# Kernel tuning notes

Measured on AMD Instinct MI355X. Metric: run time of the kernel, lower is better.

Reference implementation:

```python
import jax, jax.numpy as jnp
import numpy as np

DIM = 768
N_HEAD = 12
HEAD_DIM = 64
INNER = N_HEAD * HEAD_DIM
SCALE = HEAD_DIM ** -0.5


def setup_inputs() -> dict:
    key = jax.random.key(0)
    ks = jax.random.split(key, 12)
    B, Sf, St = 4, 2048, 2048
    from_tensor = jax.random.normal(ks[0], (B, Sf, DIM), dtype=jnp.float32)
    to_tensor = jax.random.normal(ks[1], (B, St, DIM), dtype=jnp.float32)
    attention_mask = jax.random.randint(ks[2], (B, Sf, St), 0, 2, dtype=jnp.int32)
    # Dense layers: kernel ~ RandomNormal (stddev 0.05, keras default), bias zeros
    def kern(k, fan_in, fan_out):
        return 0.05 * jax.random.normal(k, (fan_in, fan_out), dtype=jnp.float32)
    return {
        "from_tensor": from_tensor,
        "to_tensor": to_tensor,
        "attention_mask": attention_mask,
        "Wq": kern(ks[3], DIM, INNER), "bq": jnp.zeros((INNER,), jnp.float32),
        "Wk": kern(ks[4], DIM, INNER), "bk": jnp.zeros((INNER,), jnp.float32),
        "Wv": kern(ks[5], DIM, INNER), "bv": jnp.zeros((INNER,), jnp.float32),
        "Wo": kern(ks[6], INNER, DIM), "bo": jnp.zeros((DIM,), jnp.float32),
    }


def reference(from_tensor, to_tensor, attention_mask, Wq, bq, Wk, bk, Wv, bv, Wo, bo):
    B, Sf, _ = from_tensor.shape
    St = to_tensor.shape[1]
    # projections -> [B, S, n_head, head_dim] -> [B, n_head, S, head_dim]
    def split_heads(x, S):
        return x.reshape(B, S, N_HEAD, HEAD_DIM).transpose(0, 2, 1, 3)
    q = split_heads(from_tensor @ Wq + bq, Sf) * SCALE
    k = split_heads(to_tensor @ Wk + bk, St)
    v = split_heads(to_tensor @ Wv + bv, St)
    # scores [B, H, Sf, St]
    scores = jnp.einsum('bhik,bhjk->bhij', q, k)
    adder = (1.0 - attention_mask.astype(jnp.float32)) * -10000.0
    scores = scores + adder[:, None, :, :]
    probs = jax.nn.softmax(scores, axis=-1)
    out = jnp.einsum('bhij,bhjk->bhik', probs, v)  # [B, H, Sf, Dh]
    out = out.transpose(0, 2, 1, 3).reshape(B, Sf, INNER)
    return out @ Wo + bo
```

## Files before the change

### kernel.cpp

```cpp
#include <hip/hip_runtime.h>
#include <stdint.h>

#define DIM 768
#define NH 12
#define HD 64
#define BSZ 4
#define SEQ 2048
#define MROWS (BSZ*SEQ)

typedef __attribute__((ext_vector_type(8))) short v8s;
typedef __attribute__((ext_vector_type(4))) float v4f;
typedef __attribute__((ext_vector_type(8))) _Float16 v8h;
typedef __attribute__((ext_vector_type(2))) __fp16 v2fp;

__device__ __forceinline__ uint16_t f2bf(float x) {
  union { float f; uint32_t u; } v; v.f = x;
  uint32_t r = v.u + 0x7fffu + ((v.u >> 16) & 1u);
  return (uint16_t)(r >> 16);
}

#if __has_builtin(__builtin_amdgcn_cvt_pk_bf16_f32)
typedef __attribute__((ext_vector_type(2))) __bf16 v2bf;
__device__ __forceinline__ uint32_t pack_bf16(float a, float b) {
  union { v2bf v; uint32_t u; } c;
  c.v = __builtin_amdgcn_cvt_pk_bf16_f32(a, b);
  return c.u;
}
#else
__device__ __forceinline__ uint32_t pack_bf16(float a, float b) {
  return (uint32_t)f2bf(a) | ((uint32_t)f2bf(b) << 16);
}
#endif

__device__ __forceinline__ uint32_t pack_f16(float a, float b) {
#if __has_builtin(__builtin_amdgcn_cvt_pkrtz)
  union { v2fp h; uint32_t u; } c;
  c.h = __builtin_amdgcn_cvt_pkrtz(a, b);
  return c.u;
#else
  union { _Float16 h[2]; uint32_t u; } c;
  c.h[0] = (_Float16)a; c.h[1] = (_Float16)b; return c.u;
#endif
}

__device__ __forceinline__ float fexp2(float x) {
#if __has_builtin(__builtin_amdgcn_exp2f)
  return __builtin_amdgcn_exp2f(x);
#else
  return exp2f(x);
#endif
}

__device__ __forceinline__ void gl16(const void* g, void* l) {
  __builtin_amdgcn_global_load_lds(
      (const __attribute__((address_space(1))) unsigned int*)g,
      (__attribute__((address_space(3))) unsigned int*)l, 16, 0, 0);
}

__global__ void cvt_bf16_kernel(const float* __restrict__ src0, uint16_t* __restrict__ dst0,
                                const float* __restrict__ src1, uint16_t* __restrict__ dst1,
                                int n4) {
  int i = blockIdx.x * blockDim.x + threadIdx.x;
  const float* src = (i < n4) ? src0 : src1;
  uint16_t* dst = (i < n4) ? dst0 : dst1;
  int j = (i < n4) ? i : i - n4;
  float4 v = ((const float4*)src)[j];
  ushort4 o;
  o.x = f2bf(v.x); o.y = f2bf(v.y); o.z = f2bf(v.z); o.w = f2bf(v.w);
  ((ushort4*)dst)[j] = o;
}

__global__ void mask_bits_kernel(const int* __restrict__ src,
                                 unsigned long long* __restrict__ dst, int nwords) {
  int gtid = blockIdx.x * blockDim.x + threadIdx.x;
  int w = gtid >> 6;
  int lane = threadIdx.x & 63;
  if (w >= nwords) return;
  int b  = w >> 16;
  int q  = (w >> 5) & 2047;
  int kt = w & 31;
  int m = src[((size_t)b * SEQ + q) * SEQ + kt * 64 + lane];
  unsigned long long bits = __ballot(m != 0);
  if (lane == 0) dst[((size_t)b * 32 + kt) * SEQ + q] = bits;
}

__global__ void wtrans_kernel(const float* __restrict__ Wq, const float* __restrict__ Wk,
                              const float* __restrict__ Wv, const float* __restrict__ Wo,
                              uint16_t* __restrict__ WT) {
  __shared__ float tile[32][33];
  int z = blockIdx.z;
  const float* src = (z==0) ? Wq : (z==1) ? Wk : (z==2) ? Wv : Wo;
  uint16_t* dst = WT + (size_t)z * DIM * DIM;
  int tx = threadIdx.x, ty = threadIdx.y;
  int x  = blockIdx.x * 32 + tx;
  int y0 = blockIdx.y * 32;
  for (int j = ty; j < 32; j += 8)
    tile[j][tx] = src[(size_t)(y0 + j) * DIM + x];
  __syncthreads();
  int xo = y0 + tx;
  for (int j = ty; j < 32; j += 8)
    dst[(size_t)(blockIdx.x * 32 + j) * DIM + xo] = f2bf(tile[tx][j]);
}

__global__ __launch_bounds__(256) void gemm_kernel(
    const uint16_t* __restrict__ Xf, const uint16_t* __restrict__ Xt,
    const uint16_t* __restrict__ WT, const uint16_t* __restrict__ AO,
    const float* __restrict__ bq, const float* __restrict__ bk,
    const float* __restrict__ bv, const float* __restrict__ bo,
    uint16_t* __restrict__ Qw, uint16_t* __restrict__ Kw, uint16_t* __restrict__ Vw,
    float* __restrict__ Out, int mode_base)
{
  __shared__ alignas(16) uint16_t As[128 * 32];
  __shared__ alignas(16) uint16_t Bs[128 * 32];
  int mode = mode_base + blockIdx.z;
  const uint16_t* A = (mode == 0) ? Xf : (mode == 3 ? AO : Xt);
  const uint16_t* W = WT + (size_t)mode * DIM * DIM;
  const float* bias = (mode == 0) ? bq : (mode == 1) ? bk : (mode == 2) ? bv : bo;

  int m0 = blockIdx.x * 128, n0 = blockIdx.y * 128;
  int tid = threadIdx.x;
  int wave = tid >> 6, lane = tid & 63, lr = lane & 15, quad = lane >> 4;
  int wm = (wave >> 1) * 64, wn = (wave & 1) * 64;

  int seg = (lane & 3) ^ ((lane >> 3) & 3);
  const uint16_t* agl = A + (size_t)(m0 + wave * 32 + (lane >> 2)) * DIM + seg * 8;
  const uint16_t* bgl = W + (size_t)(n0 + wave * 32 + (lane >> 2)) * DIM + seg * 8;
  int lb = wave * 1024;
  int ck = (lr >> 1) & 3;

  v4f acc[4][4];
  v4f vz = {0.f, 0.f, 0.f, 0.f};
  #pragma unroll
  for (int i = 0; i < 4; i++)
    #pragma unroll
    for (int j = 0; j < 4; j++) acc[i][j] = vz;

  for (int k0 = 0; k0 < DIM; k0 += 32) {
    __syncthreads();
    gl16(agl + k0,            &As[lb]);
    gl16(agl + k0 + 16 * DIM, &As[lb + 512]);
    gl16(bgl + k0,            &Bs[lb]);
    gl16(bgl + k0 + 16 * DIM, &Bs[lb + 512]);
    __syncthreads();
    v8s af[4], bfr[4];
    #pragma unroll
    for (int i = 0; i < 4; i++)
      af[i] = *(const v8s*)&As[(wm + i * 16 + lr) * 32 + ((quad ^ ck) << 3)];
    #pragma unroll
    for (int j = 0; j < 4; j++)
      bfr[j] = *(const v8s*)&Bs[(wn + j * 16 + lr) * 32 + ((quad ^ ck) << 3)];
    #pragma unroll
    for (int i = 0; i < 4; i++)
      #pragma unroll
      for (int j = 0; j < 4; j++)
        acc[i][j] = __builtin_amdgcn_mfma_f32_16x16x32_bf16(af[i], bfr[j], acc[i][j], 0, 0, 0);
  }

  float bj[4];
  #pragma unroll
  for (int j = 0; j < 4; j++) bj[j] = bias[n0 + wn + j * 16 + lr];

  if (mode == 3) {
    #pragma unroll
    for (int i = 0; i < 4; i++) {
      int m = m0 + wm + i * 16 + quad * 4;
      #pragma unroll
      for (int j = 0; j < 4; j++) {
        int n = n0 + wn + j * 16 + lr;
        #pragma unroll
        for (int r = 0; r < 4; r++)
          Out[(size_t)(m + r) * DIM + n] = acc[i][j][r] + bj[j];
      }
    }
  } else if (mode == 2) {
    #pragma unroll
    for (int i = 0; i < 4; i++) {
      int m = m0 + wm + i * 16 + quad * 4;
      int b = m >> 11, s0 = m & 2047;
      int kk0 = s0 & 63;
      int pos = (kk0 >> 5) * 32 + ((kk0 >> 2) & 3) * 8 + ((kk0 >> 4) & 1) * 4;
      int chunk = pos >> 3, off = pos & 7;
      #pragma unroll
      for (int j = 0; j < 4; j++) {
        int n = n0 + wn + j * 16 + lr;
        int h = n >> 6, d = n & 63;
        uint2 pk;
        pk.x = pack_f16(acc[i][j][0] + bj[j], acc[i][j][1] + bj[j]);
        pk.y = pack_f16(acc[i][j][2] + bj[j], acc[i][j][3] + bj[j]);
        int idx = (s0 & ~63) + ((chunk ^ (d & 7)) << 3) + off;
        *(uint2*)&Vw[((size_t)(b * NH + h) * HD + d) * SEQ + idx] = pk;
      }
    }
  } else {
    uint16_t* Dst = (mode == 0) ? Qw : Kw;
    float scale = (mode == 0) ? 0.18033688f : 1.0f;
    #pragma unroll
    for (int i = 0; i < 4; i++) {
      int m = m0 + wm + i * 16 + quad * 4;
      int b = m >> 11, s0 = m & 2047;
      #pragma unroll
      for (int j = 0; j < 4; j++) {
        int n = n0 + wn + j * 16 + lr;
        int h = n >> 6, d = n & 63;
        #pragma unroll
        for (int r = 0; r < 4; r++) {
          float v = (acc[i][j][r] + bj[j]) * scale;
          int s = s0 + r;
          int dd = (mode == 1) ? ((((d >> 3) ^ (s & 7)) << 3) + (d & 7)) : d;
          Dst[((size_t)(b * NH + h) * SEQ + s) * HD + dd] = f2bf(v);
        }
      }
    }
  }
}

__device__ __forceinline__ void softmax8(unsigned long long mw, int sh0,
                                         const v4f* s, v8h* pf, float& lsum) {
  uint32_t mlo = (uint32_t)mw, mhi = (uint32_t)(mw >> 32);
  #pragma unroll
  for (int p = 0; p < 2; p++) {
    float ps[8];
    #pragma unroll
    for (int half = 0; half < 2; half++) {
      int nt = p * 2 + half;
      uint32_t b4 = ((nt < 2 ? mlo : mhi) >> (sh0 + ((nt & 1) << 4))) & 15u;
      #pragma unroll
      for (int r = 0; r < 4; r++) {
        float v = fexp2(s[nt][r] - 8.0f) * (float)((b4 >> r) & 1u);
        ps[half * 4 + r] = v;
        lsum += v;
      }
    }
    union { uint4 u; v8h h; } cc;
    cc.u.x = pack_f16(ps[0], ps[1]);
    cc.u.y = pack_f16(ps[2], ps[3]);
    cc.u.z = pack_f16(ps[4], ps[5]);
    cc.u.w = pack_f16(ps[6], ps[7]);
    pf[p] = cc.h;
  }
}

__global__ __launch_bounds__(128, 3) void flash_kernel(
    const uint16_t* __restrict__ Qg, const uint16_t* __restrict__ Kg,
    const uint16_t* __restrict__ Vg, const unsigned long long* __restrict__ Mb,
    uint16_t* __restrict__ AO)
{
  __shared__ alignas(16) uint16_t Ks[64 * 64];
  __shared__ alignas(16) uint16_t Vs[64 * 64];

  int tid = threadIdx.x, wave = tid >> 6, lane = tid & 63, lr = lane & 15, quad = lane >> 4;
  int bh = blockIdx.y;
  int b = bh / NH, h = bh - b * NH;
  int q0 = blockIdx.x * 64;
  const uint16_t* Qp = Qg + (size_t)bh * SEQ * HD;
  const uint16_t* Kp = Kg + (size_t)bh * SEQ * HD;
  const uint16_t* Vp = Vg + (size_t)bh * HD * SEQ;
  int qg0 = q0 + wave * 32 + lr;
  int qg1 = qg0 + 16;
  const unsigned long long* Mp0 = Mb + (size_t)b * 32 * SEQ + qg0;
  const unsigned long long* Mp1 = Mp0 + 16;

  int swk = lr & 7, sh0 = quad * 4;

  v8s qf0a = *(const v8s*)&Qp[(size_t)qg0 * HD + quad * 8];
  v8s qf0b = *(const v8s*)&Qp[(size_t)qg0 * HD + 32 + quad * 8];
  v8s qf1a = *(const v8s*)&Qp[(size_t)qg1 * HD + quad * 8];
  v8s qf1b = *(const v8s*)&Qp[(size_t)qg1 * HD + 32 + quad * 8];

  const uint16_t* kgl = Kp + ((size_t)(wave * 32 + (lane >> 3)) * HD + (lane & 7) * 8);
  const uint16_t* vgl = Vp + ((size_t)(wave * 32 + (lane >> 3)) * SEQ + (lane & 7) * 8);
  int lb = wave * 2048;

  v4f acc0[4], acc1[4];
  v4f vz = {0.f, 0.f, 0.f, 0.f};
  #pragma unroll
  for (int dt = 0; dt < 4; dt++) { acc0[dt] = vz; acc1[dt] = vz; }
  float ls0 = 0.f, ls1 = 0.f;

  for (int k0 = 0; k0 < SEQ; k0 += 64) {
    __syncthreads();
    #pragma unroll
    for (int c = 0; c < 4; c++) {
      gl16(kgl + ((size_t)k0 + c * 8) * HD, &Ks[lb + c * 512]);
      gl16(vgl + k0 + (size_t)c * 8 * SEQ, &Vs[lb + c * 512]);
    }
    unsigned long long mw0 = Mp0[(size_t)(k0 >> 6) * SEQ];
    unsigned long long mw1 = Mp1[(size_t)(k0 >> 6) * SEQ];
    __syncthreads();

    v4f s0[4], s1[4];
    #pragma unroll
    for (int nt = 0; nt < 4; nt++) {
      int rowb = (nt * 16 + lr) << 6;
      v8s kf0 = *(const v8s*)&Ks[rowb + ((quad ^ swk) << 3)];
      v8s kf1 = *(const v8s*)&Ks[rowb + (((quad + 4) ^ swk) << 3)];
      v4f z = vz;
      z = __builtin_amdgcn_mfma_f32_16x16x32_bf16(kf0, qf0a, z, 0, 0, 0);
      z = __builtin_amdgcn_mfma_f32_16x16x32_bf16(kf1, qf0b, z, 0, 0, 0);
      s0[nt] = z;
      z = vz;
      z = __builtin_amdgcn_mfma_f32_16x16x32_bf16(kf0, qf1a, z, 0, 0, 0);
      z = __builtin_amdgcn_mfma_f32_16x16x32_bf16(kf1, qf1b, z, 0, 0, 0);
      s1[nt] = z;
    }

    v8h pf0[2], pf1[2];
    softmax8(mw0, sh0, s0, pf0, ls0);
    softmax8(mw1, sh0, s1, pf1, ls1);

    #pragma unroll
    for (int dt = 0; dt < 4; dt++) {
      int rowb = (dt * 16 + lr) << 6;
      #pragma unroll
      for (int p = 0; p < 2; p++) {
        v8h vv = *(const v8h*)&Vs[rowb + (((p * 4 + quad) ^ swk) << 3)];
        acc0[dt] = __builtin_amdgcn_mfma_f32_16x16x32_f16(vv, pf0[p], acc0[dt], 0, 0, 0);
        acc1[dt] = __builtin_amdgcn_mfma_f32_16x16x32_f16(vv, pf1[p], acc1[dt], 0, 0, 0);
      }
    }
  }

  ls0 += __shfl_xor(ls0, 16); ls0 += __shfl_xor(ls0, 32);
  ls1 += __shfl_xor(ls1, 16); ls1 += __shfl_xor(ls1, 32);
  float ri0 = 1.0f / ls0, ri1 = 1.0f / ls1;

  #pragma unroll
  for (int dt = 0; dt < 4; dt++) {
    uint2 pk;
    pk.x = pack_bf16(acc0[dt][0] * ri0, acc0[dt][1] * ri0);
    pk.y = pack_bf16(acc0[dt][2] * ri0, acc0[dt][3] * ri0);
    *(uint2*)&AO[(size_t)(b * SEQ + qg0) * DIM + h * HD + dt * 16 + sh0] = pk;
    pk.x = pack_bf16(acc1[dt][0] * ri1, acc1[dt][1] * ri1);
    pk.y = pack_bf16(acc1[dt][2] * ri1, acc1[dt][3] * ri1);
    *(uint2*)&AO[(size_t)(b * SEQ + qg1) * DIM + h * HD + dt * 16 + sh0] = pk;
  }
}

extern "C" void kernel_launch(void* const* d_in, const int* in_sizes, int n_in,
                              void* d_out, int out_size, void* d_ws, size_t ws_size,
                              hipStream_t stream) {
  const float* from_t = (const float*)d_in[0];
  const float* to_t   = (const float*)d_in[1];
  const int*   maski  = (const int*)d_in[2];
  const float* Wq = (const float*)d_in[3];  const float* bq = (const float*)d_in[4];
  const float* Wk = (const float*)d_in[5];  const float* bk = (const float*)d_in[6];
  const float* Wv = (const float*)d_in[7];  const float* bv = (const float*)d_in[8];
  const float* Wo = (const float*)d_in[9];  const float* bo = (const float*)d_in[10];

  char* ws = (char*)d_ws;
  size_t off = 0;
  uint16_t* Xf = (uint16_t*)(ws + off); off += (size_t)MROWS * DIM * 2;
  uint16_t* Xt = (uint16_t*)(ws + off); off += (size_t)MROWS * DIM * 2;
  uint16_t* WT = (uint16_t*)(ws + off); off += (size_t)4 * DIM * DIM * 2;
  unsigned long long* Mbits = (unsigned long long*)(ws + off);
  off += (size_t)BSZ * 32 * SEQ * 8;
  uint16_t* Qw = (uint16_t*)(ws + off); off += (size_t)MROWS * DIM * 2;
  uint16_t* Kw = (uint16_t*)(ws + off); off += (size_t)MROWS * DIM * 2;
  uint16_t* Vw = (uint16_t*)(ws + off); off += (size_t)MROWS * DIM * 2;
  uint16_t* AO = (uint16_t*)(ws + off); off += (size_t)MROWS * DIM * 2;
  float* Out = (float*)d_out;

  int nx4 = MROWS * DIM / 4;
  cvt_bf16_kernel<<<2 * nx4 / 256, 256, 0, stream>>>(from_t, Xf, to_t, Xt, nx4);
  int nwords = BSZ * 32 * SEQ;
  mask_bits_kernel<<<nwords * 64 / 256, 256, 0, stream>>>(maski, Mbits, nwords);
  wtrans_kernel<<<dim3(24, 24, 4), dim3(32, 8), 0, stream>>>(Wq, Wk, Wv, Wo, WT);

  gemm_kernel<<<dim3(64, 6, 3), 256, 0, stream>>>(Xf, Xt, WT, AO, bq, bk, bv, bo,
                                                  Qw, Kw, Vw, Out, 0);
  flash_kernel<<<dim3(SEQ / 64, BSZ * NH), 128, 0, stream>>>(Qw, Kw, Vw, Mbits, AO);
  gemm_kernel<<<dim3(64, 6, 1), 256, 0, stream>>>(Xf, Xt, WT, AO, bq, bk, bv, bo,
                                                  Qw, Kw, Vw, Out, 3);
}
```

Before: 329.3 us.

## Transpose GEMM MFMA for vectorized epilogue stores and move row-sum to MFMA

Q/K and output projections swap MFMA operand order so each lane holds four consecutive columns, enabling float4 output stores and packed bf16 stores instead of scalar writes; the V projection is split into its own kernel keeping the old layout. In the flash kernel, the mask is applied via sign-extended bitfield AND instead of a float multiply, the softmax row sum is computed by an extra MFMA against a ones vector instead of scalar adds and shuffles, the next mask word is prefetched a tile ahead, and LDS offsets are hoisted. The prefetch reads one word past the end, so the mask workspace is enlarged; the extra MFMAs add matrix-core work.

```diff
diff --git a/kernel.cpp b/kernel.cpp
--- a/kernel.cpp
+++ b/kernel.cpp
@@ -49,6 +49,17 @@
 #else
   return exp2f(x);
 #endif
+}
+
+__device__ __forceinline__ int sbfe1(uint32_t w, int off) {
+#if __has_builtin(__builtin_amdgcn_sbfe)
+  return __builtin_amdgcn_sbfe((int)w, off, 1);
+#else
+  return ((int)(w << (31 - off))) >> 31;
+#endif
+}
+__device__ __forceinline__ float maskf(float x, int mext) {
+  union { float f; int i; } u; u.f = x; u.i &= mext; return u.f;
 }
 
 __device__ __forceinline__ void gl16(const void* g, void* l) {
@@ -102,12 +113,12 @@
     dst[(size_t)(blockIdx.x * 32 + j) * DIM + xo] = f2bf(tile[tx][j]);
 }
 
-__global__ __launch_bounds__(256) void gemm_kernel(
+__global__ __launch_bounds__(256) void gemm_t_kernel(
     const uint16_t* __restrict__ Xf, const uint16_t* __restrict__ Xt,
     const uint16_t* __restrict__ WT, const uint16_t* __restrict__ AO,
     const float* __restrict__ bq, const float* __restrict__ bk,
-    const float* __restrict__ bv, const float* __restrict__ bo,
-    uint16_t* __restrict__ Qw, uint16_t* __restrict__ Kw, uint16_t* __restrict__ Vw,
+    const float* __restrict__ bo,
+    uint16_t* __restrict__ Qw, uint16_t* __restrict__ Kw,
     float* __restrict__ Out, int mode_base)
 {
   __shared__ alignas(16) uint16_t As[128 * 32];
@@ -115,7 +126,7 @@
   int mode = mode_base + blockIdx.z;
   const uint16_t* A = (mode == 0) ? Xf : (mode == 3 ? AO : Xt);
   const uint16_t* W = WT + (size_t)mode * DIM * DIM;
-  const float* bias = (mode == 0) ? bq : (mode == 1) ? bk : (mode == 2) ? bv : bo;
+  const float* bias = (mode == 0) ? bq : (mode == 1) ? bk : bo;
 
   int m0 = blockIdx.x * 128, n0 = blockIdx.y * 128;
   int tid = threadIdx.x;
@@ -131,9 +142,9 @@
   v4f acc[4][4];
   v4f vz = {0.f, 0.f, 0.f, 0.f};
   #pragma unroll
-  for (int i = 0; i < 4; i++)
-    #pragma unroll
-    for (int j = 0; j < 4; j++) acc[i][j] = vz;
+  for (int j = 0; j < 4; j++)
+    #pragma unroll
+    for (int i = 0; i < 4; i++) acc[j][i] = vz;
 
   for (int k0 = 0; k0 < DIM; k0 += 32) {
     __syncthreads();
@@ -150,6 +161,86 @@
     for (int j = 0; j < 4; j++)
       bfr[j] = *(const v8s*)&Bs[(wn + j * 16 + lr) * 32 + ((quad ^ ck) << 3)];
     #pragma unroll
+    for (int j = 0; j < 4; j++)
+      #pragma unroll
+      for (int i = 0; i < 4; i++)
+        acc[j][i] = __builtin_amdgcn_mfma_f32_16x16x32_bf16(bfr[j], af[i], acc[j][i], 0, 0, 0);
+  }
+
+  #pragma unroll
+  for (int j = 0; j < 4; j++) {
+    int nb = n0 + wn + j * 16 + quad * 4;
+    float4 bj4 = *(const float4*)&bias[nb];
+    #pragma unroll
+    for (int i = 0; i < 4; i++) {
+      int m = m0 + wm + i * 16 + lr;
+      float v0 = acc[j][i][0] + bj4.x;
+      float v1 = acc[j][i][1] + bj4.y;
+      float v2 = acc[j][i][2] + bj4.z;
+      float v3 = acc[j][i][3] + bj4.w;
+      if (mode == 3) {
+        float4 o = {v0, v1, v2, v3};
+        *(float4*)&Out[(size_t)m * DIM + nb] = o;
+      } else {
+        if (mode == 0) {
+          v0 *= 0.18033688f; v1 *= 0.18033688f;
+          v2 *= 0.18033688f; v3 *= 0.18033688f;
+        }
+        int h = nb >> 6, d = nb & 63;
+        int b = m >> 11, s = m & 2047;
+        int dd = (mode == 1) ? ((((d >> 3) ^ (s & 7)) << 3) + (d & 7)) : d;
+        uint2 pk;
+        pk.x = pack_bf16(v0, v1);
+        pk.y = pack_bf16(v2, v3);
+        uint16_t* Dst = (mode == 0) ? Qw : Kw;
+        *(uint2*)&Dst[((size_t)(b * NH + h) * SEQ + s) * HD + dd] = pk;
+      }
+    }
+  }
+}
+
+__global__ __launch_bounds__(256) void gemm_v_kernel(
+    const uint16_t* __restrict__ Xt, const uint16_t* __restrict__ WT,
+    const float* __restrict__ bv, uint16_t* __restrict__ Vw)
+{
+  __shared__ alignas(16) uint16_t As[128 * 32];
+  __shared__ alignas(16) uint16_t Bs[128 * 32];
+  const uint16_t* A = Xt;
+  const uint16_t* W = WT + (size_t)2 * DIM * DIM;
+
+  int m0 = blockIdx.x * 128, n0 = blockIdx.y * 128;
+  int tid = threadIdx.x;
+  int wave = tid >> 6, lane = tid & 63, lr = lane & 15, quad = lane >> 4;
+  int wm = (wave >> 1) * 64, wn = (wave & 1) * 64;
+
+  int seg = (lane & 3) ^ ((lane >> 3) & 3);
+  const uint16_t* agl = A + (size_t)(m0 + wave * 32 + (lane >> 2)) * DIM + seg * 8;
+  const uint16_t* bgl = W + (size_t)(n0 + wave * 32 + (lane >> 2)) * DIM + seg * 8;
+  int lb = wave * 1024;
+  int ck = (lr >> 1) & 3;
+
+  v4f acc[4][4];
+  v4f vz = {0.f, 0.f, 0.f, 0.f};
+  #pragma unroll
+  for (int i = 0; i < 4; i++)
+    #pragma unroll
+    for (int j = 0; j < 4; j++) acc[i][j] = vz;
+
+  for (int k0 = 0; k0 < DIM; k0 += 32) {
+    __syncthreads();
+    gl16(agl + k0,            &As[lb]);
+    gl16(agl + k0 + 16 * DIM, &As[lb + 512]);
+    gl16(bgl + k0,            &Bs[lb]);
+    gl16(bgl + k0 + 16 * DIM, &Bs[lb + 512]);
+    __syncthreads();
+    v8s af[4], bfr[4];
+    #pragma unroll
+    for (int i = 0; i < 4; i++)
+      af[i] = *(const v8s*)&As[(wm + i * 16 + lr) * 32 + ((quad ^ ck) << 3)];
+    #pragma unroll
+    for (int j = 0; j < 4; j++)
+      bfr[j] = *(const v8s*)&Bs[(wn + j * 16 + lr) * 32 + ((quad ^ ck) << 3)];
+    #pragma unroll
     for (int i = 0; i < 4; i++)
       #pragma unroll
       for (int j = 0; j < 4; j++)
@@ -158,64 +249,30 @@
 
   float bj[4];
   #pragma unroll
-  for (int j = 0; j < 4; j++) bj[j] = bias[n0 + wn + j * 16 + lr];
-
-  if (mode == 3) {
-    #pragma unroll
-    for (int i = 0; i < 4; i++) {
-      int m = m0 + wm + i * 16 + quad * 4;
-      #pragma unroll
-      for (int j = 0; j < 4; j++) {
-        int n = n0 + wn + j * 16 + lr;
-        #pragma unroll
-        for (int r = 0; r < 4; r++)
-          Out[(size_t)(m + r) * DIM + n] = acc[i][j][r] + bj[j];
-      }
-    }
-  } else if (mode == 2) {
-    #pragma unroll
-    for (int i = 0; i < 4; i++) {
-      int m = m0 + wm + i * 16 + quad * 4;
-      int b = m >> 11, s0 = m & 2047;
-      int kk0 = s0 & 63;
-      int pos = (kk0 >> 5) * 32 + ((kk0 >> 2) & 3) * 8 + ((kk0 >> 4) & 1) * 4;
-      int chunk = pos >> 3, off = pos & 7;
-      #pragma unroll
-      for (int j = 0; j < 4; j++) {
-        int n = n0 + wn + j * 16 + lr;
-        int h = n >> 6, d = n & 63;
-        uint2 pk;
-        pk.x = pack_f16(acc[i][j][0] + bj[j], acc[i][j][1] + bj[j]);
-        pk.y = pack_f16(acc[i][j][2] + bj[j], acc[i][j][3] + bj[j]);
-        int idx = (s0 & ~63) + ((chunk ^ (d & 7)) << 3) + off;
-        *(uint2*)&Vw[((size_t)(b * NH + h) * HD + d) * SEQ + idx] = pk;
-      }
-    }
-  } else {
-    uint16_t* Dst = (mode == 0) ? Qw : Kw;
-    float scale = (mode == 0) ? 0.18033688f : 1.0f;
-    #pragma unroll
-    for (int i = 0; i < 4; i++) {
-      int m = m0 + wm + i * 16 + quad * 4;
-      int b = m >> 11, s0 = m & 2047;
-      #pragma unroll
-      for (int j = 0; j < 4; j++) {
-        int n = n0 + wn + j * 16 + lr;
-        int h = n >> 6, d = n & 63;
-        #pragma unroll
-        for (int r = 0; r < 4; r++) {
-          float v = (acc[i][j][r] + bj[j]) * scale;
-          int s = s0 + r;
-          int dd = (mode == 1) ? ((((d >> 3) ^ (s & 7)) << 3) + (d & 7)) : d;
-          Dst[((size_t)(b * NH + h) * SEQ + s) * HD + dd] = f2bf(v);
-        }
-      }
+  for (int j = 0; j < 4; j++) bj[j] = bv[n0 + wn + j * 16 + lr];
+
+  #pragma unroll
+  for (int i = 0; i < 4; i++) {
+    int m = m0 + wm + i * 16 + quad * 4;
+    int b = m >> 11, s0 = m & 2047;
+    int kk0 = s0 & 63;
+    int pos = (kk0 >> 5) * 32 + ((kk0 >> 2) & 3) * 8 + ((kk0 >> 4) & 1) * 4;
+    int chunk = pos >> 3, off = pos & 7;
+    #pragma unroll
+    for (int j = 0; j < 4; j++) {
+      int n = n0 + wn + j * 16 + lr;
+      int h = n >> 6, d = n & 63;
+      uint2 pk;
+      pk.x = pack_f16(acc[i][j][0] + bj[j], acc[i][j][1] + bj[j]);
+      pk.y = pack_f16(acc[i][j][2] + bj[j], acc[i][j][3] + bj[j]);
+      int idx = (s0 & ~63) + ((chunk ^ (d & 7)) << 3) + off;
+      *(uint2*)&Vw[((size_t)(b * NH + h) * HD + d) * SEQ + idx] = pk;
     }
   }
 }
 
 __device__ __forceinline__ void softmax8(unsigned long long mw, int sh0,
-                                         const v4f* s, v8h* pf, float& lsum) {
+                                         const v4f* s, v8h* pf) {
   uint32_t mlo = (uint32_t)mw, mhi = (uint32_t)(mw >> 32);
   #pragma unroll
   for (int p = 0; p < 2; p++) {
@@ -223,12 +280,12 @@
     #pragma unroll
     for (int half = 0; half < 2; half++) {
       int nt = p * 2 + half;
-      uint32_t b4 = ((nt < 2 ? mlo : mhi) >> (sh0 + ((nt & 1) << 4))) & 15u;
+      uint32_t w = (nt < 2) ? mlo : mhi;
+      int base = sh0 + ((nt & 1) << 4);
       #pragma unroll
       for (int r = 0; r < 4; r++) {
-        float v = fexp2(s[nt][r] - 8.0f) * (float)((b4 >> r) & 1u);
-        ps[half * 4 + r] = v;
-        lsum += v;
+        float e = fexp2(s[nt][r] - 8.0f);
+        ps[half * 4 + r] = maskf(e, sbfe1(w, base + r));
       }
     }
     union { uint4 u; v8h h; } cc;
@@ -271,11 +328,27 @@
   const uint16_t* vgl = Vp + ((size_t)(wave * 32 + (lane >> 3)) * SEQ + (lane & 7) * 8);
   int lb = wave * 2048;
 
-  v4f acc0[4], acc1[4];
+  int koff[4][2], voff[4][2];
+  #pragma unroll
+  for (int nt = 0; nt < 4; nt++) {
+    int rowb = (nt * 16 + lr) << 6;
+    koff[nt][0] = rowb + ((quad ^ swk) << 3);
+    koff[nt][1] = rowb + (((quad + 4) ^ swk) << 3);
+    voff[nt][0] = rowb + ((quad ^ swk) << 3);
+    voff[nt][1] = rowb + (((quad + 4) ^ swk) << 3);
+  }
+
+  v8h ones;
+  #pragma unroll
+  for (int e = 0; e < 8; e++) ones[e] = (_Float16)1.0f;
+
+  v4f acc0[4], acc1[4], accs0, accs1;
   v4f vz = {0.f, 0.f, 0.f, 0.f};
   #pragma unroll
   for (int dt = 0; dt < 4; dt++) { acc0[dt] = vz; acc1[dt] = vz; }
-  float ls0 = 0.f, ls1 = 0.f;
+  accs0 = vz; accs1 = vz;
+
+  unsigned long long nm0 = Mp0[0], nm1 = Mp1[0];
 
   for (int k0 = 0; k0 < SEQ; k0 += 64) {
     __syncthreads();
@@ -284,16 +357,16 @@
       gl16(kgl + ((size_t)k0 + c * 8) * HD, &Ks[lb + c * 512]);
       gl16(vgl + k0 + (size_t)c * 8 * SEQ, &Vs[lb + c * 512]);
     }
-    unsigned long long mw0 = Mp0[(size_t)(k0 >> 6) * SEQ];
-    unsigned long long mw1 = Mp1[(size_t)(k0 >> 6) * SEQ];
+    unsigned long long mw0 = nm0, mw1 = nm1;
+    size_t nidx = (size_t)((k0 >> 6) + 1) * SEQ;
+    nm0 = Mp0[nidx]; nm1 = Mp1[nidx];
     __syncthreads();
 
     v4f s0[4], s1[4];
     #pragma unroll
     for (int nt = 0; nt < 4; nt++) {
-      int rowb = (nt * 16 + lr) << 6;
-      v8s kf0 = *(const v8s*)&Ks[rowb + ((quad ^ swk) << 3)];
-      v8s kf1 = *(const v8s*)&Ks[rowb + (((quad + 4) ^ swk) << 3)];
+      v8s kf0 = *(const v8s*)&Ks[koff[nt][0]];
+      v8s kf1 = *(const v8s*)&Ks[koff[nt][1]];
       v4f z = vz;
       z = __builtin_amdgcn_mfma_f32_16x16x32_bf16(kf0, qf0a, z, 0, 0, 0);
       z = __builtin_amdgcn_mfma_f32_16x16x32_bf16(kf1, qf0b, z, 0, 0, 0);
@@ -305,24 +378,27 @@
     }
 
     v8h pf0[2], pf1[2];
-    softmax8(mw0, sh0, s0, pf0, ls0);
-    softmax8(mw1, sh0, s1, pf1, ls1);
+    softmax8(mw0, sh0, s0, pf0);
+    softmax8(mw1, sh0, s1, pf1);
 
     #pragma unroll
     for (int dt = 0; dt < 4; dt++) {
-      int rowb = (dt * 16 + lr) << 6;
       #pragma unroll
       for (int p = 0; p < 2; p++) {
-        v8h vv = *(const v8h*)&Vs[rowb + (((p * 4 + quad) ^ swk) << 3)];
+        v8h vv = *(const v8h*)&Vs[voff[dt][p]];
         acc0[dt] = __builtin_amdgcn_mfma_f32_16x16x32_f16(vv, pf0[p], acc0[dt], 0, 0, 0);
         acc1[dt] = __builtin_amdgcn_mfma_f32_16x16x32_f16(vv, pf1[p], acc1[dt], 0, 0, 0);
       }
     }
-  }
-
-  ls0 += __shfl_xor(ls0, 16); ls0 += __shfl_xor(ls0, 32);
-  ls1 += __shfl_xor(ls1, 16); ls1 += __shfl_xor(ls1, 32);
-  float ri0 = 1.0f / ls0, ri1 = 1.0f / ls1;
+    #pragma unroll
+    for (int p = 0; p < 2; p++) {
+      accs0 = __builtin_amdgcn_mfma_f32_16x16x32_f16(ones, pf0[p], accs0, 0, 0, 0);
+      accs1 = __builtin_amdgcn_mfma_f32_16x16x32_f16(ones, pf1[p], accs1, 0, 0, 0);
+    }
+  }
+
+  float ri0 = 1.0f / accs0[0];
+  float ri1 = 1.0f / accs1[0];
 
   #pragma unroll
   for (int dt = 0; dt < 4; dt++) {
@@ -353,7 +429,7 @@
   uint16_t* Xt = (uint16_t*)(ws + off); off += (size_t)MROWS * DIM * 2;
   uint16_t* WT = (uint16_t*)(ws + off); off += (size_t)4 * DIM * DIM * 2;
   unsigned long long* Mbits = (unsigned long long*)(ws + off);
-  off += (size_t)BSZ * 32 * SEQ * 8;
+  off += (size_t)(BSZ * 32 + 1) * SEQ * 8;
   uint16_t* Qw = (uint16_t*)(ws + off); off += (size_t)MROWS * DIM * 2;
   uint16_t* Kw = (uint16_t*)(ws + off); off += (size_t)MROWS * DIM * 2;
   uint16_t* Vw = (uint16_t*)(ws + off); off += (size_t)MROWS * DIM * 2;
@@ -366,9 +442,10 @@
   mask_bits_kernel<<<nwords * 64 / 256, 256, 0, stream>>>(maski, Mbits, nwords);
   wtrans_kernel<<<dim3(24, 24, 4), dim3(32, 8), 0, stream>>>(Wq, Wk, Wv, Wo, WT);
 
-  gemm_kernel<<<dim3(64, 6, 3), 256, 0, stream>>>(Xf, Xt, WT, AO, bq, bk, bv, bo,
-                                                  Qw, Kw, Vw, Out, 0);
+  gemm_t_kernel<<<dim3(64, 6, 2), 256, 0, stream>>>(Xf, Xt, WT, AO, bq, bk, bo,
+                                                    Qw, Kw, Out, 0);
+  gemm_v_kernel<<<dim3(64, 6), 256, 0, stream>>>(Xt, WT, bv, Vw);
   flash_kernel<<<dim3(SEQ / 64, BSZ * NH), 128, 0, stream>>>(Qw, Kw, Vw, Mbits, AO);
-  gemm_kernel<<<dim3(64, 6, 1), 256, 0, stream>>>(Xf, Xt, WT, AO, bq, bk, bv, bo,
-                                                  Qw, Kw, Vw, Out, 3);
-}
+  gemm_t_kernel<<<dim3(64, 6, 1), 256, 0, stream>>>(Xf, Xt, WT, AO, bq, bk, bo,
+                                                    Qw, Kw, Out, 3);
+}
```

New measurement: 333.9 us. About the same (+1.4%).
